# Performance work log

Measured on AMD Instinct MI355X. Metric: run time of the kernel, lower is better.

Reference implementation:

```python
import jax, jax.numpy as jnp
import numpy as np

N_NODES = 100000
N_EDGES = 1600000


def setup_inputs() -> dict:
    key = jax.random.key(0)
    k1, k2, k3, k4, k5 = jax.random.split(key, 5)
    node_states = jax.random.normal(k1, (N_NODES, 128), dtype=jnp.float32)
    edge_index = jax.random.randint(k2, (2, N_EDGES), 0, N_NODES, dtype=jnp.int64)
    mask = jax.random.uniform(k3, (N_EDGES,), dtype=jnp.float32)  # edge weights
    # Glorot-ish init for the two GCN linear layers
    W1 = jax.random.normal(k4, (128, 64), dtype=jnp.float32) * 0.05
    b1 = jnp.zeros((64,), dtype=jnp.float32)
    W2 = jax.random.normal(k5, (64, 64), dtype=jnp.float32) * 0.05
    b2 = jnp.zeros((64,), dtype=jnp.float32)
    return {"node_states": node_states, "edge_index": edge_index, "mask": mask,
            "W1": W1, "b1": b1, "W2": W2, "b2": b2}


def _gcn_layer(x, src, dst, edge_w, W, b, n_nodes):
    # PyG GCNConv (normalize=False): h = x @ W; out[dst] += edge_w * h[src]; out += b
    h = x @ W                                  # [N, d_out]
    msg = h[src] * edge_w[:, None]             # [E, d_out] gather + scale
    agg = jax.ops.segment_sum(msg, dst, num_segments=n_nodes)  # scatter-add
    return agg + b


def reference(node_states, edge_index, mask, W1, b1, W2, b2):
    src = edge_index[0]
    dst = edge_index[1]
    n = node_states.shape[0]
    h1 = jax.nn.relu(_gcn_layer(node_states, src, dst, mask, W1, b1, n))
    h2 = jax.nn.relu(_gcn_layer(h1, src, dst, mask, W2, b2, n))
    return h2
```

## Files before the change

kernel.cpp:

```cpp
#include <hip/hip_runtime.h>
#include <hip/hip_bf16.h>

#define N_NODES 100000
#define N_EDGES 1600000
#define NBUCKET 391
#define NBLK 640
#define CHUNK_E 2500
#define CAP 4608
#define GCSTRIDE 32

typedef short v8s __attribute__((ext_vector_type(8)));
typedef float v4f __attribute__((ext_vector_type(4)));

static __device__ __forceinline__ unsigned pack_bf2(float a, float b) {
    __hip_bfloat162 p = __float22bfloat162_rn(make_float2(a, b));
    return *reinterpret_cast<unsigned*>(&p);
}
static __device__ __forceinline__ float2 bf2_to_f2(unsigned u) {
    __hip_bfloat162 p = *reinterpret_cast<__hip_bfloat162*>(&u);
    return __bfloat1622float2(p);
}

template<int K, bool IN_BF>
static __device__ __forceinline__ void gemm_tile(const void* __restrict__ in,
                                                 const float* __restrict__ W,
                                                 unsigned* __restrict__ outp,
                                                 int tile, unsigned* smem) {
    unsigned (*xs)[K / 2 + 4] = (unsigned(*)[K / 2 + 4])smem;
    unsigned (*ws)[K / 2 + 4] = (unsigned(*)[K / 2 + 4])(smem + 64 * (K / 2 + 4));
    const int t = threadIdx.x;
    const int row0 = tile * 64;
    {
        const float2* g2 = (const float2*)W;
        for (int i = t; i < 64 * K / 2; i += 256) {
            const float2 v = g2[i];
            const int k = (2 * i) >> 6;
            const int c = (2 * i) & 63;
            ((short*)&ws[c][0])[k]     = (short)(pack_bf2(v.x, 0.f) & 0xFFFF);
            ((short*)&ws[c + 1][0])[k] = (short)(pack_bf2(v.y, 0.f) & 0xFFFF);
        }
    }
    if (IN_BF) {
        const uint2* g = (const uint2*)in;
        for (int i = t; i < 64 * K / 4; i += 256) {
            const int r = i / (K / 4), cu = i % (K / 4);
            const int row = row0 + r;
            uint2 v = make_uint2(0u, 0u);
            if (row < N_NODES) v = g[(size_t)row * (K / 4) + cu];
            ((uint2*)&xs[r][0])[cu] = v;
        }
    } else {
        const float4* g = (const float4*)in;
        for (int i = t; i < 64 * K / 4; i += 256) {
            const int r = i / (K / 4), cu = i % (K / 4);
            const int row = row0 + r;
            uint2 v = make_uint2(0u, 0u);
            if (row < N_NODES) {
                float4 f = g[(size_t)row * (K / 4) + cu];
                v.x = pack_bf2(f.x, f.y);
                v.y = pack_bf2(f.z, f.w);
            }
            ((uint2*)&xs[r][0])[cu] = v;
        }
    }
    __syncthreads();
    const int w = t >> 6;
    const int lane = t & 63;
    const int l15 = lane & 15;
    const int quad = lane >> 4;
    v4f acc[4];
#pragma unroll
    for (int tt = 0; tt < 4; ++tt) acc[tt] = (v4f){0.f, 0.f, 0.f, 0.f};
#pragma unroll
    for (int k0 = 0; k0 < K; k0 += 32) {
        const int ku = k0 / 2 + quad * 4;
        const v8s xb = *(const v8s*)&xs[w * 16 + l15][ku];
#pragma unroll
        for (int tt = 0; tt < 4; ++tt) {
            const v8s wa = *(const v8s*)&ws[16 * tt + l15][ku];
            acc[tt] = __builtin_amdgcn_mfma_f32_16x16x32_bf16(wa, xb, acc[tt], 0, 0, 0);
        }
    }
    const int node = row0 + w * 16 + l15;
    if (node < N_NODES) {
#pragma unroll
        for (int tt = 0; tt < 4; ++tt) {
            uint2 o;
            o.x = pack_bf2(acc[tt][0], acc[tt][1]);
            o.y = pack_bf2(acc[tt][2], acc[tt][3]);
            *(uint2*)&outp[(size_t)node * 32 + 8 * tt + 2 * quad] = o;
        }
    }
}

__global__ __launch_bounds__(256) void k1_sort_gemm(const int* __restrict__ src,
                                                    const int* __restrict__ dst,
                                                    const float* __restrict__ wgt,
                                                    const float* __restrict__ x,
                                                    const float* __restrict__ W1,
                                                    int* __restrict__ gcount,
                                                    int2* __restrict__ arena,
                                                    unsigned* __restrict__ hpre) {
    __shared__ unsigned smem[2 * 64 * (128 / 2 + 4)];
    __shared__ int hist[NBUCKET];
    __shared__ int cur[NBUCKET];
    const int b = blockIdx.x;
    if (b >= NBLK) {
        gemm_tile<128, false>(x, W1, hpre, b - NBLK, smem);
        return;
    }
    const int t = threadIdx.x;
    for (int i = t; i < NBUCKET; i += 256) hist[i] = 0;
    __syncthreads();
    const int4* d4 = (const int4*)(dst + b * CHUNK_E);
    for (int i = t; i < CHUNK_E / 4; i += 256) {
        const int4 v = d4[i];
        atomicAdd(&hist[v.x >> 8], 1);
        atomicAdd(&hist[v.y >> 8], 1);
        atomicAdd(&hist[v.z >> 8], 1);
        atomicAdd(&hist[v.w >> 8], 1);
    }
    __syncthreads();
    for (int i = t; i < NBUCKET; i += 256) {
        const int h = hist[i];
        const int base = (h > 0) ? atomicAdd(&gcount[i * GCSTRIDE], h) : 0;
        cur[i] = i * CAP + base;
    }
    __syncthreads();
    const int4*   s4p = (const int4*)(src + b * CHUNK_E);
    const float4* w4  = (const float4*)(wgt + b * CHUNK_E);
    for (int i = t; i < CHUNK_E / 4; i += 256) {
        const int4 sv = s4p[i];
        const int4 dv = d4[i];
        const float4 wv = w4[i];
        {
            const int pos = atomicAdd(&cur[dv.x >> 8], 1);
            arena[pos] = make_int2(sv.x | ((dv.x & 255) << 17), __float_as_int(wv.x));
        }
        {
            const int pos = atomicAdd(&cur[dv.y >> 8], 1);
            arena[pos] = make_int2(sv.y | ((dv.y & 255) << 17), __float_as_int(wv.y));
        }
        {
            const int pos = atomicAdd(&cur[dv.z >> 8], 1);
            arena[pos] = make_int2(sv.z | ((dv.z & 255) << 17), __float_as_int(wv.z));
        }
        {
            const int pos = atomicAdd(&cur[dv.w >> 8], 1);
            arena[pos] = make_int2(sv.w | ((dv.w & 255) << 17), __float_as_int(wv.w));
        }
    }
}

__global__ __launch_bounds__(256) void gemm2_k(const unsigned* __restrict__ h1bf,
                                               const float* __restrict__ W2,
                                               unsigned* __restrict__ hpre) {
    __shared__ unsigned smem[2 * 64 * (64 / 2 + 4)];
    gemm_tile<64, true>(h1bf, W2, hpre, blockIdx.x, smem);
}

__global__ __launch_bounds__(256) void s4_fine(const int2* __restrict__ arena,
                                               const int* __restrict__ gcount,
                                               unsigned* __restrict__ edge_sorted,
                                               int* __restrict__ row_ptr) {
    __shared__ int hist[256];
    __shared__ int part[256];
    __shared__ int cursor[256];
    __shared__ int sb[2];
    const int b = blockIdx.x;
    const int t = threadIdx.x;
    int partial = 0;
    for (int i = t; i < b; i += 256) partial += gcount[i * GCSTRIDE];
    part[t] = partial;
    __syncthreads();
    for (int off = 128; off > 0; off >>= 1) {
        if (t < off) part[t] += part[t + off];
        __syncthreads();
    }
    if (t == 0) { sb[0] = part[0]; sb[1] = gcount[b * GCSTRIDE]; }
    __syncthreads();
    const int gbase = sb[0];
    const int cnt   = sb[1];
    const int abeg  = b * CAP;
    hist[t] = 0;
    __syncthreads();
    for (int i = t; i < cnt; i += 256)
        atomicAdd(&hist[(arena[abeg + i].x >> 17) & 255], 1);
    __syncthreads();
    const int v = hist[t];
    part[t] = v;
    __syncthreads();
    for (int off = 1; off < 256; off <<= 1) {
        int u = (t >= off) ? part[t - off] : 0;
        __syncthreads();
        part[t] += u;
        __syncthreads();
    }
    const int excl = gbase + part[t] - v;
    cursor[t] = excl;
    const int node = b * 256 + t;
    if (node < N_NODES) row_ptr[node] = excl;
    if (b == NBUCKET - 1 && t == 0) row_ptr[N_NODES] = N_EDGES;
    __syncthreads();
    for (int i = t; i < cnt; i += 256) {
        const int2 ev = arena[abeg + i];
        const int f = (ev.x >> 17) & 255;
        const int pos = atomicAdd(&cursor[f], 1);
        unsigned wq = (unsigned)__float2uint_rn(__int_as_float(ev.y) * 32767.f);
        wq = min(wq, 32767u);
        edge_sorted[pos] = (unsigned)(ev.x & 0x1FFFF) | (wq << 17);
    }
}

template<bool FULL>
static __device__ __forceinline__ void octo_step(const unsigned* __restrict__ h,
                                                 const unsigned* __restrict__ recs,
                                                 int e, int n, int q, int cg,
                                                 float acc[8]) {
    unsigned u;
    if (FULL) {
        u = recs[e + q];
    } else {
        u = recs[e + min(q, n - 1)];
    }
    const int sx = u & 0x1FFFF;
    float wq = (float)(u >> 17) * (1.f / 32767.f);
    if (!FULL) wq = (q < n) ? wq : 0.f;
    const uint4 hv = *(const uint4*)&h[(size_t)sx * 32 + cg * 4];
    const float2 f0 = bf2_to_f2(hv.x);
    const float2 f1 = bf2_to_f2(hv.y);
    const float2 f2 = bf2_to_f2(hv.z);
    const float2 f3 = bf2_to_f2(hv.w);
    acc[0] += wq * f0.x; acc[1] += wq * f0.y;
    acc[2] += wq * f1.x; acc[3] += wq * f1.y;
    acc[4] += wq * f2.x; acc[5] += wq * f2.y;
    acc[6] += wq * f3.x; acc[7] += wq * f3.y;
}

template<bool OUT_BF>
__global__ __launch_bounds__(256) void gather_octo(const unsigned* __restrict__ h,
                                                   const int* __restrict__ row_ptr,
                                                   const unsigned* __restrict__ recs,
                                                   const float* __restrict__ bias,
                                                   void* __restrict__ outp) {
    const int node = (blockIdx.x * 256 + threadIdx.x) >> 6;
    if (node >= N_NODES) return;
    const int lane = threadIdx.x & 63;
    const int q  = lane >> 3;
    const int cg = lane & 7;
    const int beg = __builtin_amdgcn_readfirstlane(row_ptr[node]);
    const int end = __builtin_amdgcn_readfirstlane(row_ptr[node + 1]);
    float acc[8];
#pragma unroll
    for (int i = 0; i < 8; ++i) acc[i] = 0.f;
    int e = beg;
    for (; e + 16 <= end; e += 16) {
        octo_step<true>(h, recs, e, 8, q, cg, acc);
        octo_step<true>(h, recs, e + 8, 8, q, cg, acc);
    }
    if (e + 8 <= end) {
        octo_step<true>(h, recs, e, 8, q, cg, acc);
        e += 8;
    }
    if (e < end) {
        octo_step<false>(h, recs, e, end - e, q, cg, acc);
    }
    const bool h8 = (lane & 8) != 0;
    const float t0 = __shfl_xor(h8 ? acc[0] : acc[4], 8);
    const float t1 = __shfl_xor(h8 ? acc[1] : acc[5], 8);
    const float t2 = __shfl_xor(h8 ? acc[2] : acc[6], 8);
    const float t3 = __shfl_xor(h8 ? acc[3] : acc[7], 8);
    const float a0 = (h8 ? acc[4] : acc[0]) + t0;
    const float a1 = (h8 ? acc[5] : acc[1]) + t1;
    const float a2 = (h8 ? acc[6] : acc[2]) + t2;
    const float a3 = (h8 ? acc[7] : acc[3]) + t3;
    const bool h16 = (lane & 16) != 0;
    const float u0 = __shfl_xor(h16 ? a0 : a2, 16);
    const float u1 = __shfl_xor(h16 ? a1 : a3, 16);
    const float b0 = (h16 ? a2 : a0) + u0;
    const float b1 = (h16 ? a3 : a1) + u1;
    const bool h32 = (lane & 32) != 0;
    const float v0 = __shfl_xor(h32 ? b0 : b1, 32);
    const float rsum = (h32 ? b1 : b0) + v0;
    const int colq = ((q & 1) << 2) | (q & 2) | ((q >> 2) & 1);
    const int col = 8 * cg + colq;
    const float r = fmaxf(rsum + bias[col], 0.f);
    if (OUT_BF) {
        const unsigned p = pack_bf2(r, 0.f);
        ((short*)outp)[(size_t)node * 64 + col] = (short)(p & 0xFFFF);
    } else {
        ((float*)outp)[(size_t)node * 64 + col] = r;
    }
}

extern "C" void kernel_launch(void* const* d_in, const int* in_sizes, int n_in,
                              void* d_out, int out_size, void* d_ws, size_t ws_size,
                              hipStream_t stream) {
    const float* x    = (const float*)d_in[0];
    const int*   eidx = (const int*)d_in[1];
    const float* mask = (const float*)d_in[2];
    const float* W1   = (const float*)d_in[3];
    const float* b1   = (const float*)d_in[4];
    const float* W2   = (const float*)d_in[5];
    const float* b2   = (const float*)d_in[6];
    float* out = (float*)d_out;

    const int* src = eidx;
    const int* dst = eidx + N_EDGES;

    unsigned* hpre        = (unsigned*)d_ws;
    unsigned* edge_sorted = (unsigned*)(hpre + (size_t)N_NODES * 32);
    int2*     arena       = (int2*)(edge_sorted + N_EDGES);
    unsigned* h1bf        = (unsigned*)arena;
    int*      gcount      = (int*)(arena + (size_t)NBUCKET * CAP);
    int*      row_ptr     = gcount + NBUCKET * GCSTRIDE;

    const int gemmBlocks = (N_NODES + 63) / 64;
    const int gatherBlocks = (N_NODES * 64 + 255) / 256;

    hipMemsetAsync(gcount, 0, NBUCKET * GCSTRIDE * sizeof(int), stream);

    k1_sort_gemm<<<NBLK + gemmBlocks, 256, 0, stream>>>(src, dst, mask, x, W1,
                                                        gcount, arena, hpre);
    s4_fine<<<NBUCKET, 256, 0, stream>>>(arena, gcount, edge_sorted, row_ptr);

    gather_octo<true><<<gatherBlocks, 256, 0, stream>>>(hpre, row_ptr, edge_sorted,
                                                        b1, h1bf);
    gemm2_k<<<gemmBlocks, 256, 0, stream>>>(h1bf, W2, hpre);
    gather_octo<false><<<gatherBlocks, 256, 0, stream>>>(hpre, row_ptr, edge_sorted,
                                                         b2, out);
}
```

Measured before the change: 253.2 us.

## Stage bucketed edges in LDS before coalesced arena writes; widen blocks to 1024

The coarse bucket pass now does a local prefix sum over bucket counts, places each edge in its bucket order in shared memory, then writes the arena in a second pass. This replaces scattered global stores from shared-counter atomics with writes that are contiguous per bucket. The sort, fine-sort and layer-1 GEMM kernels move to 1024-thread blocks, so each GEMM block now has 16 waves computing one 16x16 output tile each instead of 4 waves computing four. The price is more barriers, heavier LDS use per block (about 36 KB) and possibly lower occupancy.

```diff
diff --git a/kernel.cpp b/kernel.cpp
--- a/kernel.cpp
+++ b/kernel.cpp
@@ -21,18 +21,154 @@
     return __bfloat1622float2(p);
 }
 
-template<int K, bool IN_BF>
-static __device__ __forceinline__ void gemm_tile(const void* __restrict__ in,
-                                                 const float* __restrict__ W,
-                                                 unsigned* __restrict__ outp,
-                                                 int tile, unsigned* smem) {
-    unsigned (*xs)[K / 2 + 4] = (unsigned(*)[K / 2 + 4])smem;
-    unsigned (*ws)[K / 2 + 4] = (unsigned(*)[K / 2 + 4])(smem + 64 * (K / 2 + 4));
+__global__ __launch_bounds__(1024) void k1_sort_gemm(const int* __restrict__ src,
+                                                     const int* __restrict__ dst,
+                                                     const float* __restrict__ wgt,
+                                                     const float* __restrict__ x,
+                                                     const float* __restrict__ W1,
+                                                     int* __restrict__ gcount,
+                                                     int2* __restrict__ arena,
+                                                     unsigned* __restrict__ hpre) {
+    __shared__ unsigned smem[9216];
+    const int b = blockIdx.x;
     const int t = threadIdx.x;
-    const int row0 = tile * 64;
+
+    if (b >= NBLK) {
+        unsigned (*xs)[68] = (unsigned(*)[68])smem;
+        unsigned (*ws)[68] = (unsigned(*)[68])(smem + 64 * 68);
+        const int tile = b - NBLK;
+        const int row0 = tile * 64;
+        {
+            const float2* g2 = (const float2*)W1;
+            for (int i = t; i < 64 * 128 / 2; i += 1024) {
+                const float2 v = g2[i];
+                const int k = (2 * i) >> 6;
+                const int c = (2 * i) & 63;
+                ((short*)&ws[c][0])[k]     = (short)(pack_bf2(v.x, 0.f) & 0xFFFF);
+                ((short*)&ws[c + 1][0])[k] = (short)(pack_bf2(v.y, 0.f) & 0xFFFF);
+            }
+        }
+        {
+            const float4* g = (const float4*)x;
+            for (int i = t; i < 64 * 32; i += 1024) {
+                const int r = i >> 5, cu = i & 31;
+                const int row = row0 + r;
+                uint2 v = make_uint2(0u, 0u);
+                if (row < N_NODES) {
+                    float4 f = g[(size_t)row * 32 + cu];
+                    v.x = pack_bf2(f.x, f.y);
+                    v.y = pack_bf2(f.z, f.w);
+                }
+                ((uint2*)&xs[r][0])[cu] = v;
+            }
+        }
+        __syncthreads();
+        const int w = t >> 6, lane = t & 63;
+        const int l15 = lane & 15, quad = lane >> 4;
+        const int a = w & 3;
+        const int g_ = w >> 2;
+        v4f acc = (v4f){0.f, 0.f, 0.f, 0.f};
+#pragma unroll
+        for (int k0 = 0; k0 < 128; k0 += 32) {
+            const int ku = k0 / 2 + quad * 4;
+            const v8s xb = *(const v8s*)&xs[g_ * 16 + l15][ku];
+            const v8s wa = *(const v8s*)&ws[16 * a + l15][ku];
+            acc = __builtin_amdgcn_mfma_f32_16x16x32_bf16(wa, xb, acc, 0, 0, 0);
+        }
+        const int node = row0 + g_ * 16 + l15;
+        if (node < N_NODES) {
+            uint2 o;
+            o.x = pack_bf2(acc[0], acc[1]);
+            o.y = pack_bf2(acc[2], acc[3]);
+            *(uint2*)&hpre[(size_t)node * 32 + 8 * a + 2 * quad] = o;
+        }
+        return;
+    }
+
+    int*  hist = (int*)smem;
+    int*  part = (int*)smem + 400;
+    int*  lcur = (int*)smem + 912;
+    int*  tgb  = (int*)smem + 1304;
+    int2* ord  = (int2*)((int*)smem + 1696);
+    int*  tg   = (int*)smem + 1696 + 5000;
+
+    for (int i = t; i < NBUCKET; i += 1024) hist[i] = 0;
+    __syncthreads();
+    const int4* d4 = (const int4*)(dst + b * CHUNK_E);
+    for (int i = t; i < CHUNK_E / 4; i += 1024) {
+        const int4 v = d4[i];
+        atomicAdd(&hist[v.x >> 8], 1);
+        atomicAdd(&hist[v.y >> 8], 1);
+        atomicAdd(&hist[v.z >> 8], 1);
+        atomicAdd(&hist[v.w >> 8], 1);
+    }
+    __syncthreads();
+    if (t < 512) part[t] = (t < NBUCKET) ? hist[t] : 0;
+    __syncthreads();
+    for (int off = 1; off < 512; off <<= 1) {
+        int u = 0;
+        if (t < 512 && t >= off) u = part[t - off];
+        __syncthreads();
+        if (t < 512) part[t] += u;
+        __syncthreads();
+    }
+    if (t < NBUCKET) {
+        const int hv = hist[t];
+        const int lbase = part[t] - hv;
+        lcur[t] = lbase;
+        int grsv = 0;
+        if (hv > 0) grsv = atomicAdd(&gcount[t * GCSTRIDE], hv);
+        tgb[t] = t * CAP + grsv - lbase;
+    }
+    __syncthreads();
+    const int4*   s4p = (const int4*)(src + b * CHUNK_E);
+    const float4* w4  = (const float4*)(wgt + b * CHUNK_E);
+    for (int i = t; i < CHUNK_E / 4; i += 1024) {
+        const int4 sv = s4p[i];
+        const int4 dv = d4[i];
+        const float4 wv = w4[i];
+        {
+            const int bk = dv.x >> 8;
+            const int lp = atomicAdd(&lcur[bk], 1);
+            ord[lp] = make_int2(sv.x | ((dv.x & 255) << 17), __float_as_int(wv.x));
+            tg[lp] = tgb[bk] + lp;
+        }
+        {
+            const int bk = dv.y >> 8;
+            const int lp = atomicAdd(&lcur[bk], 1);
+            ord[lp] = make_int2(sv.y | ((dv.y & 255) << 17), __float_as_int(wv.y));
+            tg[lp] = tgb[bk] + lp;
+        }
+        {
+            const int bk = dv.z >> 8;
+            const int lp = atomicAdd(&lcur[bk], 1);
+            ord[lp] = make_int2(sv.z | ((dv.z & 255) << 17), __float_as_int(wv.z));
+            tg[lp] = tgb[bk] + lp;
+        }
+        {
+            const int bk = dv.w >> 8;
+            const int lp = atomicAdd(&lcur[bk], 1);
+            ord[lp] = make_int2(sv.w | ((dv.w & 255) << 17), __float_as_int(wv.w));
+            tg[lp] = tgb[bk] + lp;
+        }
+    }
+    __syncthreads();
+    for (int i = t; i < CHUNK_E; i += 1024) {
+        arena[tg[i]] = ord[i];
+    }
+}
+
+__global__ __launch_bounds__(256) void gemm2_k(const unsigned* __restrict__ in,
+                                               const float* __restrict__ W2,
+                                               unsigned* __restrict__ outp) {
+    __shared__ unsigned smem[2 * 64 * 36];
+    unsigned (*xs)[36] = (unsigned(*)[36])smem;
+    unsigned (*ws)[36] = (unsigned(*)[36])(smem + 64 * 36);
+    const int t = threadIdx.x;
+    const int row0 = blockIdx.x * 64;
     {
-        const float2* g2 = (const float2*)W;
-        for (int i = t; i < 64 * K / 2; i += 256) {
+        const float2* g2 = (const float2*)W2;
+        for (int i = t; i < 64 * 64 / 2; i += 256) {
             const float2 v = g2[i];
             const int k = (2 * i) >> 6;
             const int c = (2 * i) & 63;
@@ -40,39 +176,24 @@
             ((short*)&ws[c + 1][0])[k] = (short)(pack_bf2(v.y, 0.f) & 0xFFFF);
         }
     }
-    if (IN_BF) {
+    {
         const uint2* g = (const uint2*)in;
-        for (int i = t; i < 64 * K / 4; i += 256) {
-            const int r = i / (K / 4), cu = i % (K / 4);
+        for (int i = t; i < 64 * 16; i += 256) {
+            const int r = i >> 4, cu = i & 15;
             const int row = row0 + r;
             uint2 v = make_uint2(0u, 0u);
-            if (row < N_NODES) v = g[(size_t)row * (K / 4) + cu];
+            if (row < N_NODES) v = g[(size_t)row * 16 + cu];
             ((uint2*)&xs[r][0])[cu] = v;
         }
-    } else {
-        const float4* g = (const float4*)in;
-        for (int i = t; i < 64 * K / 4; i += 256) {
-            const int r = i / (K / 4), cu = i % (K / 4);
-            const int row = row0 + r;
-            uint2 v = make_uint2(0u, 0u);
-            if (row < N_NODES) {
-                float4 f = g[(size_t)row * (K / 4) + cu];
-                v.x = pack_bf2(f.x, f.y);
-                v.y = pack_bf2(f.z, f.w);
-            }
-            ((uint2*)&xs[r][0])[cu] = v;
-        }
-    }
-    __syncthreads();
-    const int w = t >> 6;
-    const int lane = t & 63;
-    const int l15 = lane & 15;
-    const int quad = lane >> 4;
+    }
+    __syncthreads();
+    const int w = t >> 6, lane = t & 63;
+    const int l15 = lane & 15, quad = lane >> 4;
     v4f acc[4];
 #pragma unroll
     for (int tt = 0; tt < 4; ++tt) acc[tt] = (v4f){0.f, 0.f, 0.f, 0.f};
 #pragma unroll
-    for (int k0 = 0; k0 < K; k0 += 32) {
+    for (int k0 = 0; k0 < 64; k0 += 32) {
         const int ku = k0 / 2 + quad * 4;
         const v8s xb = *(const v8s*)&xs[w * 16 + l15][ku];
 #pragma unroll
@@ -93,116 +214,51 @@
     }
 }
 
-__global__ __launch_bounds__(256) void k1_sort_gemm(const int* __restrict__ src,
-                                                    const int* __restrict__ dst,
-                                                    const float* __restrict__ wgt,
-                                                    const float* __restrict__ x,
-                                                    const float* __restrict__ W1,
-                                                    int* __restrict__ gcount,
-                                                    int2* __restrict__ arena,
-                                                    unsigned* __restrict__ hpre) {
-    __shared__ unsigned smem[2 * 64 * (128 / 2 + 4)];
-    __shared__ int hist[NBUCKET];
-    __shared__ int cur[NBUCKET];
-    const int b = blockIdx.x;
-    if (b >= NBLK) {
-        gemm_tile<128, false>(x, W1, hpre, b - NBLK, smem);
-        return;
-    }
-    const int t = threadIdx.x;
-    for (int i = t; i < NBUCKET; i += 256) hist[i] = 0;
-    __syncthreads();
-    const int4* d4 = (const int4*)(dst + b * CHUNK_E);
-    for (int i = t; i < CHUNK_E / 4; i += 256) {
-        const int4 v = d4[i];
-        atomicAdd(&hist[v.x >> 8], 1);
-        atomicAdd(&hist[v.y >> 8], 1);
-        atomicAdd(&hist[v.z >> 8], 1);
-        atomicAdd(&hist[v.w >> 8], 1);
-    }
-    __syncthreads();
-    for (int i = t; i < NBUCKET; i += 256) {
-        const int h = hist[i];
-        const int base = (h > 0) ? atomicAdd(&gcount[i * GCSTRIDE], h) : 0;
-        cur[i] = i * CAP + base;
-    }
-    __syncthreads();
-    const int4*   s4p = (const int4*)(src + b * CHUNK_E);
-    const float4* w4  = (const float4*)(wgt + b * CHUNK_E);
-    for (int i = t; i < CHUNK_E / 4; i += 256) {
-        const int4 sv = s4p[i];
-        const int4 dv = d4[i];
-        const float4 wv = w4[i];
-        {
-            const int pos = atomicAdd(&cur[dv.x >> 8], 1);
-            arena[pos] = make_int2(sv.x | ((dv.x & 255) << 17), __float_as_int(wv.x));
-        }
-        {
-            const int pos = atomicAdd(&cur[dv.y >> 8], 1);
-            arena[pos] = make_int2(sv.y | ((dv.y & 255) << 17), __float_as_int(wv.y));
-        }
-        {
-            const int pos = atomicAdd(&cur[dv.z >> 8], 1);
-            arena[pos] = make_int2(sv.z | ((dv.z & 255) << 17), __float_as_int(wv.z));
-        }
-        {
-            const int pos = atomicAdd(&cur[dv.w >> 8], 1);
-            arena[pos] = make_int2(sv.w | ((dv.w & 255) << 17), __float_as_int(wv.w));
-        }
-    }
-}
-
-__global__ __launch_bounds__(256) void gemm2_k(const unsigned* __restrict__ h1bf,
-                                               const float* __restrict__ W2,
-                                               unsigned* __restrict__ hpre) {
-    __shared__ unsigned smem[2 * 64 * (64 / 2 + 4)];
-    gemm_tile<64, true>(h1bf, W2, hpre, blockIdx.x, smem);
-}
-
-__global__ __launch_bounds__(256) void s4_fine(const int2* __restrict__ arena,
-                                               const int* __restrict__ gcount,
-                                               unsigned* __restrict__ edge_sorted,
-                                               int* __restrict__ row_ptr) {
+__global__ __launch_bounds__(1024) void s4_fine(const int2* __restrict__ arena,
+                                                const int* __restrict__ gcount,
+                                                unsigned* __restrict__ edge_sorted,
+                                                int* __restrict__ row_ptr) {
+    __shared__ int red[1024];
     __shared__ int hist[256];
     __shared__ int part[256];
     __shared__ int cursor[256];
-    __shared__ int sb[2];
     const int b = blockIdx.x;
     const int t = threadIdx.x;
     int partial = 0;
-    for (int i = t; i < b; i += 256) partial += gcount[i * GCSTRIDE];
-    part[t] = partial;
-    __syncthreads();
-    for (int off = 128; off > 0; off >>= 1) {
-        if (t < off) part[t] += part[t + off];
-        __syncthreads();
-    }
-    if (t == 0) { sb[0] = part[0]; sb[1] = gcount[b * GCSTRIDE]; }
-    __syncthreads();
-    const int gbase = sb[0];
-    const int cnt   = sb[1];
+    for (int i = t; i < b; i += 1024) partial += gcount[i * GCSTRIDE];
+    red[t] = partial;
+    __syncthreads();
+    for (int off = 512; off > 0; off >>= 1) {
+        if (t < off) red[t] += red[t + off];
+        __syncthreads();
+    }
+    const int gbase = red[0];
+    const int cnt   = gcount[b * GCSTRIDE];
     const int abeg  = b * CAP;
-    hist[t] = 0;
-    __syncthreads();
-    for (int i = t; i < cnt; i += 256)
+    if (t < 256) hist[t] = 0;
+    __syncthreads();
+    for (int i = t; i < cnt; i += 1024)
         atomicAdd(&hist[(arena[abeg + i].x >> 17) & 255], 1);
     __syncthreads();
-    const int v = hist[t];
-    part[t] = v;
+    const int v = (t < 256) ? hist[t] : 0;
+    if (t < 256) part[t] = v;
     __syncthreads();
     for (int off = 1; off < 256; off <<= 1) {
-        int u = (t >= off) ? part[t - off] : 0;
-        __syncthreads();
-        part[t] += u;
-        __syncthreads();
-    }
-    const int excl = gbase + part[t] - v;
-    cursor[t] = excl;
-    const int node = b * 256 + t;
-    if (node < N_NODES) row_ptr[node] = excl;
+        int u = 0;
+        if (t < 256 && t >= off) u = part[t - off];
+        __syncthreads();
+        if (t < 256) part[t] += u;
+        __syncthreads();
+    }
+    if (t < 256) {
+        const int excl = gbase + part[t] - v;
+        cursor[t] = excl;
+        const int node = b * 256 + t;
+        if (node < N_NODES) row_ptr[node] = excl;
+    }
     if (b == NBUCKET - 1 && t == 0) row_ptr[N_NODES] = N_EDGES;
     __syncthreads();
-    for (int i = t; i < cnt; i += 256) {
+    for (int i = t; i < cnt; i += 1024) {
         const int2 ev = arena[abeg + i];
         const int f = (ev.x >> 17) & 255;
         const int pos = atomicAdd(&cursor[f], 1);
@@ -320,9 +376,9 @@
 
     hipMemsetAsync(gcount, 0, NBUCKET * GCSTRIDE * sizeof(int), stream);
 
-    k1_sort_gemm<<<NBLK + gemmBlocks, 256, 0, stream>>>(src, dst, mask, x, W1,
-                                                        gcount, arena, hpre);
-    s4_fine<<<NBUCKET, 256, 0, stream>>>(arena, gcount, edge_sorted, row_ptr);
+    k1_sort_gemm<<<NBLK + gemmBlocks, 1024, 0, stream>>>(src, dst, mask, x, W1,
+                                                         gcount, arena, hpre);
+    s4_fine<<<NBUCKET, 1024, 0, stream>>>(arena, gcount, edge_sorted, row_ptr);
 
     gather_octo<true><<<gatherBlocks, 256, 0, stream>>>(hpre, row_ptr, edge_sorted,
                                                         b1, h1bf);
```

After: 239.0 us. 5.6% less time.
